# Optimization experiments

Hardware: AMD Instinct MI355X
Metric: run time of the kernel (lower is better)

Reference implementation:

```python
import jax, jax.numpy as jnp
import numpy as np
from jax import lax

NUM_CLASSES = 5  # config['training']['num_classes_per_task']
EMBED_DIM = 64


def _conv(x, w, b, pad):
    y = lax.conv_general_dilated(x, w, (1, 1), [(pad, pad), (pad, pad)],
                                 dimension_numbers=('NCHW', 'OIHW', 'NCHW'))
    return y + b[None, :, None, None]


def _maxpool2(x):
    n, c, h, w = x.shape
    return x.reshape(n, c, h // 2, 2, w // 2, 2).max(axis=(3, 5))


def _lenet(x, c1w, c1b, c2w, c2b, f1w, f1b, f2w, f2b, f3w, f3b):
    h = _maxpool2(jax.nn.relu(_conv(x, c1w, c1b, pad=2)))   # [N,6,14,14]
    h = _maxpool2(jax.nn.relu(_conv(h, c2w, c2b, pad=0)))   # [N,16,5,5]
    h = h.reshape(h.shape[0], -1)                            # [N,400]
    h = jax.nn.relu(h @ f1w.T + f1b)                         # [N,120]
    h = jax.nn.relu(h @ f2w.T + f2b)                         # [N,84]
    return h @ f3w.T + f3b                                   # [N,64]


def setup_inputs() -> dict:
    key = jax.random.key(0)
    ks = jax.random.split(key, 12)
    s = 0.1
    return {
        'x': jax.random.normal(ks[0], (20480, 1, 28, 28), dtype=jnp.float32),
        'c1w': jax.random.normal(ks[1], (6, 1, 5, 5), dtype=jnp.float32) * s,
        'c1b': jnp.zeros((6,), dtype=jnp.float32),
        'c2w': jax.random.normal(ks[2], (16, 6, 5, 5), dtype=jnp.float32) * s,
        'c2b': jnp.zeros((16,), dtype=jnp.float32),
        'f1w': jax.random.normal(ks[3], (120, 400), dtype=jnp.float32) * s,
        'f1b': jnp.zeros((120,), dtype=jnp.float32),
        'f2w': jax.random.normal(ks[4], (84, 120), dtype=jnp.float32) * s,
        'f2b': jnp.zeros((84,), dtype=jnp.float32),
        'f3w': jax.random.normal(ks[5], (EMBED_DIM, 84), dtype=jnp.float32) * s,
        'f3b': jnp.zeros((EMBED_DIM,), dtype=jnp.float32),
    }


def reference(x, c1w, c1b, c2w, c2b, f1w, f1b, f2w, f2b, f3w, f3b):
    emb = _lenet(x, c1w, c1b, c2w, c2b, f1w, f1b, f2w, f2b, f3w, f3b)  # [N,D]
    # Source builds a flat prototypes list of all N*D scalars / num_classes,
    # but only indices 0..D-1 are ever read -> first embedding row / num_classes.
    proto = emb[0] / NUM_CLASSES                     # [D]
    s = jax.nn.softmax(emb, axis=1)                  # softmax over dim 1
    # fun_L(x, p) = sqrt((x-p)^2) = |x-p|
    logits = jnp.abs(s - proto[None, :])             # [N,D]
    batch_size = x.shape[0] // NUM_CLASSES
    return logits.reshape(batch_size, NUM_CLASSES, -1)
```

## Files before the change

### kernel.cpp

```cpp
#include <hip/hip_runtime.h>


__device__ __forceinline__ int xcd_swizzle(int orig, int nwg) {
    int xcd = orig & 7, q = nwg >> 3, r = nwg & 7;
    int base = (xcd < r) ? xcd * (q + 1) : r * (q + 1) + (xcd - r) * q;
    return base + (orig >> 3);
}

__global__ __launch_bounds__(256) void transpose_x(
    const float* __restrict__ x, float* __restrict__ xt, int nc)
{
    __shared__ float t[64][65];
    const int tx = threadIdx.x & 63, ty = threadIdx.x >> 6;
    const int p0 = blockIdx.x * 64, n0 = blockIdx.y * 64;
    #pragma unroll
    for (int rr = 0; rr < 16; ++rr) {
        int nl = rr * 4 + ty;
        int pp = p0 + tx;
        int pr = pp >> 5, pc = pp & 31;
        float v = 0.f;
        if (pr >= 2 && pr < 30 && pc >= 2 && pc < 30)
            v = x[(size_t)(n0 + nl) * 784 + (pr - 2) * 28 + (pc - 2)];
        t[tx][nl] = v;
    }
    __syncthreads();
    #pragma unroll
    for (int rr = 0; rr < 16; ++rr) {
        int pl = rr * 4 + ty;
        xt[(size_t)(p0 + pl) * nc + n0 + tx] = t[pl][tx];
    }
}

__global__ __launch_bounds__(256, 1) void conv1_bt(
    const float* __restrict__ xt, const float* __restrict__ c1w,
    const float* __restrict__ c1b, float* __restrict__ p1t, int nc)
{
    const int newid = xcd_swizzle(blockIdx.x, gridDim.x);
    const int grp = newid / 196, pos = newid - grp * 196;
    const int py = pos / 14, px = pos - py * 14;
    const int img = grp * 512 + threadIdx.x * 2;
    const int pbase = (2 * py) * 32 + 2 * px;

    float2 p[36];
    #pragma unroll
    for (int r = 0; r < 6; ++r)
        #pragma unroll
        for (int cc = 0; cc < 6; ++cc)
            p[r * 6 + cc] =
                *(const float2*)&xt[(size_t)(pbase + r * 32 + cc) * nc + img];

    #pragma unroll
    for (int ch = 0; ch < 6; ++ch) {
        float w[25];
        const float* wp = c1w + ch * 25;
        #pragma unroll
        for (int k = 0; k < 25; ++k) w[k] = wp[k];
        float b = c1b[ch];
        float ma = -1e30f, mb = -1e30f;
        #pragma unroll
        for (int dy = 0; dy < 2; ++dy)
        #pragma unroll
        for (int dx = 0; dx < 2; ++dx) {
            float aa = b, ab = b;
            #pragma unroll
            for (int ky = 0; ky < 5; ++ky)
            #pragma unroll
            for (int kx = 0; kx < 5; ++kx) {
                float ww = w[ky * 5 + kx];
                float2 pv = p[(dy + ky) * 6 + dx + kx];
                aa += pv.x * ww;
                ab += pv.y * ww;
            }
            ma = fmaxf(ma, aa); mb = fmaxf(mb, ab);
        }
        float2 o2 = make_float2(fmaxf(ma, 0.f), fmaxf(mb, 0.f));
        *(float2*)&p1t[(size_t)(ch * 196 + pos) * nc + img] = o2;
    }
}

__global__ __launch_bounds__(256, 1) void conv2_bt(
    const float* __restrict__ p1t, const float* __restrict__ c2w,
    const float* __restrict__ c2b, float* __restrict__ ht, int nc)
{
    const int newid = xcd_swizzle(blockIdx.x, gridDim.x);
    const int grp = newid / 25, pos = newid - grp * 25;
    const int qy = pos / 5, qx = pos - qy * 5;
    const int img = grp * 256 + threadIdx.x;
    const int y0 = 2 * qy, x0 = 2 * qx;

    #pragma unroll 1
    for (int pass = 0; pass < 2; ++pass) {
        float acc[32];
        #pragma unroll
        for (int i = 0; i < 32; ++i) acc[i] = 0.f;

        #pragma unroll 1
        for (int ci = 0; ci < 6; ++ci) {
            float pa[36];
            #pragma unroll
            for (int r = 0; r < 6; ++r)
                #pragma unroll
                for (int cc = 0; cc < 6; ++cc)
                    pa[r * 6 + cc] =
                        p1t[(size_t)(ci * 196 + (y0 + r) * 14 + x0 + cc) * nc + img];
            #pragma unroll
            for (int o8 = 0; o8 < 8; ++o8) {
                float w[25];
                const float* wp = c2w + ((pass * 8 + o8) * 6 + ci) * 25;
                #pragma unroll
                for (int k = 0; k < 25; ++k) w[k] = wp[k];
                #pragma unroll
                for (int ky = 0; ky < 5; ++ky)
                #pragma unroll
                for (int kx = 0; kx < 5; ++kx) {
                    float ww = w[ky * 5 + kx];
                    acc[o8*4+0] += pa[ky*6+kx]       * ww;
                    acc[o8*4+1] += pa[ky*6+kx+1]     * ww;
                    acc[o8*4+2] += pa[(ky+1)*6+kx]   * ww;
                    acc[o8*4+3] += pa[(ky+1)*6+kx+1] * ww;
                }
            }
        }
        #pragma unroll
        for (int o8 = 0; o8 < 8; ++o8) {
            int oc = pass * 8 + o8;
            float b = c2b[oc];
            float m = fmaxf(fmaxf(acc[o8*4+0], acc[o8*4+1]),
                            fmaxf(acc[o8*4+2], acc[o8*4+3])) + b;
            ht[(size_t)(oc * 25 + pos) * nc + img] = fmaxf(m, 0.f);
        }
    }
}

__global__ __launch_bounds__(256) void fc1_bt(
    const float* __restrict__ ht, const float* __restrict__ f1w,
    const float* __restrict__ f1b, float* __restrict__ a1t, int nc)
{
    const int newid = xcd_swizzle(blockIdx.x, gridDim.x);
    const int grp = newid / 15, og = newid - grp * 15;
    const int img = grp * 512 + threadIdx.x * 2;
    const float* wb = f1w + og * 8 * 400;

    float2 acc[8];
    #pragma unroll
    for (int j = 0; j < 8; ++j) acc[j] = make_float2(0.f, 0.f);

    #pragma unroll 4
    for (int k = 0; k < 400; ++k) {
        float2 hv = *(const float2*)&ht[(size_t)k * nc + img];
        #pragma unroll
        for (int j = 0; j < 8; ++j) {
            float w = wb[j * 400 + k];
            acc[j].x += hv.x * w;
            acc[j].y += hv.y * w;
        }
    }
    #pragma unroll
    for (int j = 0; j < 8; ++j) {
        int o = og * 8 + j;
        float b = f1b[o];
        float2 o2 = make_float2(fmaxf(acc[j].x + b, 0.f),
                                fmaxf(acc[j].y + b, 0.f));
        *(float2*)&a1t[(size_t)o * nc + img] = o2;
    }
}

__global__ __launch_bounds__(256) void fc2_bt(
    const float* __restrict__ a1t, const float* __restrict__ f2w,
    const float* __restrict__ f2b, float* __restrict__ a2t, int nc)
{
    const int newid = xcd_swizzle(blockIdx.x, gridDim.x);
    const int grp = newid / 12, og = newid - grp * 12;
    const int img = grp * 512 + threadIdx.x * 2;
    const float* wb = f2w + og * 7 * 120;

    float2 acc[7];
    #pragma unroll
    for (int j = 0; j < 7; ++j) acc[j] = make_float2(0.f, 0.f);

    #pragma unroll 4
    for (int k = 0; k < 120; ++k) {
        float2 hv = *(const float2*)&a1t[(size_t)k * nc + img];
        #pragma unroll
        for (int j = 0; j < 7; ++j) {
            float w = wb[j * 120 + k];
            acc[j].x += hv.x * w;
            acc[j].y += hv.y * w;
        }
    }
    #pragma unroll
    for (int j = 0; j < 7; ++j) {
        int o = og * 7 + j;
        float b = f2b[o];
        float2 o2 = make_float2(fmaxf(acc[j].x + b, 0.f),
                                fmaxf(acc[j].y + b, 0.f));
        *(float2*)&a2t[(size_t)o * nc + img] = o2;
    }
}

__global__ __launch_bounds__(256) void fc3_bt(
    const float* __restrict__ a2t, const float* __restrict__ f3w,
    const float* __restrict__ f3b, float* __restrict__ embt,
    int nc, int Ntot, int n0)
{
    const int newid = xcd_swizzle(blockIdx.x, gridDim.x);
    const int grp = newid / 8, og = newid - grp * 8;
    const int limg = grp * 512 + threadIdx.x * 2;
    const float* wb = f3w + og * 8 * 84;

    float2 acc[8];
    #pragma unroll
    for (int j = 0; j < 8; ++j) acc[j] = make_float2(0.f, 0.f);

    #pragma unroll 4
    for (int k = 0; k < 84; ++k) {
        float2 hv = *(const float2*)&a2t[(size_t)k * nc + limg];
        #pragma unroll
        for (int j = 0; j < 8; ++j) {
            float w = wb[j * 84 + k];
            acc[j].x += hv.x * w;
            acc[j].y += hv.y * w;
        }
    }
    #pragma unroll
    for (int j = 0; j < 8; ++j) {
        int o = og * 8 + j;
        float b = f3b[o];
        float2 o2 = make_float2(acc[j].x + b, acc[j].y + b);
        *(float2*)&embt[(size_t)o * Ntot + n0 + limg] = o2;
    }
}

__global__ __launch_bounds__(256) void proto_head_t(
    const float* __restrict__ embt, float* __restrict__ out, int N)
{
    const int img = blockIdx.x * 256 + threadIdx.x;
    float v[64];
    float m = -1e30f;
    #pragma unroll
    for (int o = 0; o < 64; ++o) {
        v[o] = embt[(size_t)o * N + img];
        m = fmaxf(m, v[o]);
    }
    float s = 0.f;
    #pragma unroll
    for (int o = 0; o < 64; ++o) {
        v[o] = __expf(v[o] - m);
        s += v[o];
    }
    float inv = __frcp_rn(s);
    #pragma unroll
    for (int o = 0; o < 64; o += 4) {
        float4 r;
        r.x = fabsf(v[o+0] * inv - embt[(size_t)(o+0) * N] * 0.2f);
        r.y = fabsf(v[o+1] * inv - embt[(size_t)(o+1) * N] * 0.2f);
        r.z = fabsf(v[o+2] * inv - embt[(size_t)(o+2) * N] * 0.2f);
        r.w = fabsf(v[o+3] * inv - embt[(size_t)(o+3) * N] * 0.2f);
        *(float4*)&out[(size_t)img * 64 + o] = r;
    }
}

extern "C" void kernel_launch(void* const* d_in, const int* in_sizes, int n_in,
                              void* d_out, int out_size, void* d_ws, size_t ws_size,
                              hipStream_t stream)
{
    const float* x   = (const float*)d_in[0];
    const float* c1w = (const float*)d_in[1];
    const float* c1b = (const float*)d_in[2];
    const float* c2w = (const float*)d_in[3];
    const float* c2b = (const float*)d_in[4];
    const float* f1w = (const float*)d_in[5];
    const float* f1b = (const float*)d_in[6];
    const float* f2w = (const float*)d_in[7];
    const float* f2b = (const float*)d_in[8];
    const float* f3w = (const float*)d_in[9];
    const float* f3b = (const float*)d_in[10];
    float* out = (float*)d_out;

    const int N = in_sizes[0] / 784;
    float* base = (float*)d_ws;

    int c = 40;
    const int cands[] = {1, 2, 4, 5, 8, 10, 20, 40};
    for (int k = 0; k < 8; ++k) {
        int cd = cands[k];
        if (N % cd) continue;
        int ncq = N / cd;
        if (ncq % 512) continue;
        size_t need = (size_t)8800 * ncq + (size_t)256 * N;
        if (need <= ws_size) { c = cd; break; }
    }
    const int nc = N / c;

    float* xt   = base;
    float* p1t  = base + (size_t)1024 * nc;
    float* ht_  = base;
    float* a1t  = p1t;
    float* a2t  = p1t + (size_t)120 * nc;
    float* embt = base + (size_t)2200 * nc;

    for (int k = 0; k < c; ++k) {
        int n0 = k * nc;
        transpose_x<<<dim3(16, nc / 64), 256, 0, stream>>>(
            x + (size_t)n0 * 784, xt, nc);
        conv1_bt<<<196 * (nc / 512), 256, 0, stream>>>(
            xt, c1w, c1b, p1t, nc);
        conv2_bt<<<25 * (nc / 256), 256, 0, stream>>>(
            p1t, c2w, c2b, ht_, nc);
        fc1_bt<<<15 * (nc / 512), 256, 0, stream>>>(
            ht_, f1w, f1b, a1t, nc);
        fc2_bt<<<12 * (nc / 512), 256, 0, stream>>>(
            a1t, f2w, f2b, a2t, nc);
        fc3_bt<<<8 * (nc / 512), 256, 0, stream>>>(
            a2t, f3w, f3b, embt, nc, N, n0);
    }
    proto_head_t<<<N / 256, 256, 0, stream>>>(embt, out, N);
}
```

Measured before the change: 290.3 us.

## Widen conv kernels to four images per thread and split conv2 channels across blocks

conv1 and conv2 now process four images per thread with float4 loads and stores. conv1 now accumulates the four pooling positions together, adds the bias and takes the max afterwards. conv2 now splits its 16 output channels into four groups of four spread across blocks, instead of looping two passes of eight. Launch bounds change to allow up to 2 waves per EU, and the chunk-size search now requires multiples of 1024 images. The aim is wider memory transactions and more weight reuse per load, at the cost of higher register pressure and conv2 reloading its input patch once per channel group.

```diff
diff --git a/kernel.cpp b/kernel.cpp
--- a/kernel.cpp
+++ b/kernel.cpp
@@ -5,6 +5,10 @@
     int xcd = orig & 7, q = nwg >> 3, r = nwg & 7;
     int base = (xcd < r) ? xcd * (q + 1) : r * (q + 1) + (xcd - r) * q;
     return base + (orig >> 3);
+}
+
+__device__ __forceinline__ void fma4(float4& a, const float4& p, float w) {
+    a.x += p.x * w; a.y += p.y * w; a.z += p.z * w; a.w += p.w * w;
 }
 
 __global__ __launch_bounds__(256) void transpose_x(
@@ -31,23 +35,24 @@
     }
 }
 
-__global__ __launch_bounds__(256, 1) void conv1_bt(
+__global__ __launch_bounds__(256) __attribute__((amdgpu_waves_per_eu(1, 2)))
+void conv1_bt(
     const float* __restrict__ xt, const float* __restrict__ c1w,
     const float* __restrict__ c1b, float* __restrict__ p1t, int nc)
 {
     const int newid = xcd_swizzle(blockIdx.x, gridDim.x);
     const int grp = newid / 196, pos = newid - grp * 196;
     const int py = pos / 14, px = pos - py * 14;
-    const int img = grp * 512 + threadIdx.x * 2;
+    const int img = grp * 1024 + threadIdx.x * 4;
     const int pbase = (2 * py) * 32 + 2 * px;
 
-    float2 p[36];
+    float4 p[36];
     #pragma unroll
     for (int r = 0; r < 6; ++r)
         #pragma unroll
         for (int cc = 0; cc < 6; ++cc)
             p[r * 6 + cc] =
-                *(const float2*)&xt[(size_t)(pbase + r * 32 + cc) * nc + img];
+                *(const float4*)&xt[(size_t)(pbase + r * 32 + cc) * nc + img];
 
     #pragma unroll
     for (int ch = 0; ch < 6; ++ch) {
@@ -56,79 +61,81 @@
         #pragma unroll
         for (int k = 0; k < 25; ++k) w[k] = wp[k];
         float b = c1b[ch];
-        float ma = -1e30f, mb = -1e30f;
-        #pragma unroll
-        for (int dy = 0; dy < 2; ++dy)
-        #pragma unroll
-        for (int dx = 0; dx < 2; ++dx) {
-            float aa = b, ab = b;
+        float4 a00 = make_float4(0, 0, 0, 0), a01 = a00, a10 = a00, a11 = a00;
+        #pragma unroll
+        for (int ky = 0; ky < 5; ++ky)
+        #pragma unroll
+        for (int kx = 0; kx < 5; ++kx) {
+            float ww = w[ky * 5 + kx];
+            fma4(a00, p[ky * 6 + kx], ww);
+            fma4(a01, p[ky * 6 + kx + 1], ww);
+            fma4(a10, p[(ky + 1) * 6 + kx], ww);
+            fma4(a11, p[(ky + 1) * 6 + kx + 1], ww);
+        }
+        float4 o;
+        o.x = fmaxf(fmaxf(fmaxf(a00.x, a01.x), fmaxf(a10.x, a11.x)) + b, 0.f);
+        o.y = fmaxf(fmaxf(fmaxf(a00.y, a01.y), fmaxf(a10.y, a11.y)) + b, 0.f);
+        o.z = fmaxf(fmaxf(fmaxf(a00.z, a01.z), fmaxf(a10.z, a11.z)) + b, 0.f);
+        o.w = fmaxf(fmaxf(fmaxf(a00.w, a01.w), fmaxf(a10.w, a11.w)) + b, 0.f);
+        *(float4*)&p1t[(size_t)(ch * 196 + pos) * nc + img] = o;
+    }
+}
+
+__global__ __launch_bounds__(256) __attribute__((amdgpu_waves_per_eu(1, 2)))
+void conv2_bt(
+    const float* __restrict__ p1t, const float* __restrict__ c2w,
+    const float* __restrict__ c2b, float* __restrict__ ht, int nc)
+{
+    const int newid = xcd_swizzle(blockIdx.x, gridDim.x);
+    const int grp = newid / 100, rem = newid - grp * 100;
+    const int pass = rem / 25, pos = rem - pass * 25;
+    const int qy = pos / 5, qx = pos - qy * 5;
+    const int img = grp * 1024 + threadIdx.x * 4;
+    const int y0 = 2 * qy, x0 = 2 * qx;
+
+    float4 acc[16];
+    #pragma unroll
+    for (int i = 0; i < 16; ++i) acc[i] = make_float4(0, 0, 0, 0);
+
+    #pragma unroll 1
+    for (int ci = 0; ci < 6; ++ci) {
+        float4 pa[36];
+        #pragma unroll
+        for (int r = 0; r < 6; ++r)
+            #pragma unroll
+            for (int cc = 0; cc < 6; ++cc)
+                pa[r * 6 + cc] = *(const float4*)
+                    &p1t[(size_t)(ci * 196 + (y0 + r) * 14 + x0 + cc) * nc + img];
+        #pragma unroll
+        for (int o4 = 0; o4 < 4; ++o4) {
+            float w[25];
+            const float* wp = c2w + ((pass * 4 + o4) * 6 + ci) * 25;
+            #pragma unroll
+            for (int k = 0; k < 25; ++k) w[k] = wp[k];
             #pragma unroll
             for (int ky = 0; ky < 5; ++ky)
             #pragma unroll
             for (int kx = 0; kx < 5; ++kx) {
                 float ww = w[ky * 5 + kx];
-                float2 pv = p[(dy + ky) * 6 + dx + kx];
-                aa += pv.x * ww;
-                ab += pv.y * ww;
+                fma4(acc[o4 * 4 + 0], pa[ky * 6 + kx], ww);
+                fma4(acc[o4 * 4 + 1], pa[ky * 6 + kx + 1], ww);
+                fma4(acc[o4 * 4 + 2], pa[(ky + 1) * 6 + kx], ww);
+                fma4(acc[o4 * 4 + 3], pa[(ky + 1) * 6 + kx + 1], ww);
             }
-            ma = fmaxf(ma, aa); mb = fmaxf(mb, ab);
-        }
-        float2 o2 = make_float2(fmaxf(ma, 0.f), fmaxf(mb, 0.f));
-        *(float2*)&p1t[(size_t)(ch * 196 + pos) * nc + img] = o2;
-    }
-}
-
-__global__ __launch_bounds__(256, 1) void conv2_bt(
-    const float* __restrict__ p1t, const float* __restrict__ c2w,
-    const float* __restrict__ c2b, float* __restrict__ ht, int nc)
-{
-    const int newid = xcd_swizzle(blockIdx.x, gridDim.x);
-    const int grp = newid / 25, pos = newid - grp * 25;
-    const int qy = pos / 5, qx = pos - qy * 5;
-    const int img = grp * 256 + threadIdx.x;
-    const int y0 = 2 * qy, x0 = 2 * qx;
-
-    #pragma unroll 1
-    for (int pass = 0; pass < 2; ++pass) {
-        float acc[32];
-        #pragma unroll
-        for (int i = 0; i < 32; ++i) acc[i] = 0.f;
-
-        #pragma unroll 1
-        for (int ci = 0; ci < 6; ++ci) {
-            float pa[36];
-            #pragma unroll
-            for (int r = 0; r < 6; ++r)
-                #pragma unroll
-                for (int cc = 0; cc < 6; ++cc)
-                    pa[r * 6 + cc] =
-                        p1t[(size_t)(ci * 196 + (y0 + r) * 14 + x0 + cc) * nc + img];
-            #pragma unroll
-            for (int o8 = 0; o8 < 8; ++o8) {
-                float w[25];
-                const float* wp = c2w + ((pass * 8 + o8) * 6 + ci) * 25;
-                #pragma unroll
-                for (int k = 0; k < 25; ++k) w[k] = wp[k];
-                #pragma unroll
-                for (int ky = 0; ky < 5; ++ky)
-                #pragma unroll
-                for (int kx = 0; kx < 5; ++kx) {
-                    float ww = w[ky * 5 + kx];
-                    acc[o8*4+0] += pa[ky*6+kx]       * ww;
-                    acc[o8*4+1] += pa[ky*6+kx+1]     * ww;
-                    acc[o8*4+2] += pa[(ky+1)*6+kx]   * ww;
-                    acc[o8*4+3] += pa[(ky+1)*6+kx+1] * ww;
-                }
-            }
-        }
-        #pragma unroll
-        for (int o8 = 0; o8 < 8; ++o8) {
-            int oc = pass * 8 + o8;
-            float b = c2b[oc];
-            float m = fmaxf(fmaxf(acc[o8*4+0], acc[o8*4+1]),
-                            fmaxf(acc[o8*4+2], acc[o8*4+3])) + b;
-            ht[(size_t)(oc * 25 + pos) * nc + img] = fmaxf(m, 0.f);
-        }
+        }
+    }
+    #pragma unroll
+    for (int o4 = 0; o4 < 4; ++o4) {
+        int oc = pass * 4 + o4;
+        float b = c2b[oc];
+        float4 a0 = acc[o4 * 4 + 0], a1 = acc[o4 * 4 + 1];
+        float4 a2 = acc[o4 * 4 + 2], a3 = acc[o4 * 4 + 3];
+        float4 o;
+        o.x = fmaxf(fmaxf(fmaxf(a0.x, a1.x), fmaxf(a2.x, a3.x)) + b, 0.f);
+        o.y = fmaxf(fmaxf(fmaxf(a0.y, a1.y), fmaxf(a2.y, a3.y)) + b, 0.f);
+        o.z = fmaxf(fmaxf(fmaxf(a0.z, a1.z), fmaxf(a2.z, a3.z)) + b, 0.f);
+        o.w = fmaxf(fmaxf(fmaxf(a0.w, a1.w), fmaxf(a2.w, a3.w)) + b, 0.f);
+        *(float4*)&ht[(size_t)(oc * 25 + pos) * nc + img] = o;
     }
 }
 
@@ -280,13 +287,13 @@
     const int N = in_sizes[0] / 784;
     float* base = (float*)d_ws;
 
-    int c = 40;
-    const int cands[] = {1, 2, 4, 5, 8, 10, 20, 40};
-    for (int k = 0; k < 8; ++k) {
+    int c = 20;
+    const int cands[] = {1, 2, 4, 5, 10, 20};
+    for (int k = 0; k < 6; ++k) {
         int cd = cands[k];
         if (N % cd) continue;
         int ncq = N / cd;
-        if (ncq % 512) continue;
+        if (ncq % 1024) continue;
         size_t need = (size_t)8800 * ncq + (size_t)256 * N;
         if (need <= ws_size) { c = cd; break; }
     }
@@ -303,9 +310,9 @@
         int n0 = k * nc;
         transpose_x<<<dim3(16, nc / 64), 256, 0, stream>>>(
             x + (size_t)n0 * 784, xt, nc);
-        conv1_bt<<<196 * (nc / 512), 256, 0, stream>>>(
+        conv1_bt<<<196 * (nc / 1024), 256, 0, stream>>>(
             xt, c1w, c1b, p1t, nc);
-        conv2_bt<<<25 * (nc / 256), 256, 0, stream>>>(
+        conv2_bt<<<100 * (nc / 1024), 256, 0, stream>>>(
             p1t, c2w, c2b, ht_, nc);
         fc1_bt<<<15 * (nc / 512), 256, 0, stream>>>(
             ht_, f1w, f1b, a1t, nc);
```

Result: slower. 301.6 us (+3.9%).
